# Performance work log

Hardware: AMD Instinct MI355X
Metric: run time of the kernel (lower is better)

## Reference

```python
import jax, jax.numpy as jnp
import numpy as np

N_PAPER = 50000
N_AUTHOR = 50000
E = 400000
N_FEAT = 256
N_HID = 256
N_CLASS = 128
TEMP = 1.0  # cfg.temparature


def setup_inputs() -> dict:
    key = jax.random.key(0)
    ks = jax.random.split(key, 40)
    def lin_init(k, shape, fan_in):
        s = 1.0 / np.sqrt(fan_in)
        return jax.random.uniform(k, shape, jnp.float32, -s, s)
    inp = {}
    inp['x_paper'] = jax.random.normal(ks[0], (N_PAPER, N_FEAT), jnp.float32)
    # xavier-uniform embedding for featureless node type 'author'
    xs = np.sqrt(6.0 / (N_AUTHOR + N_FEAT))
    inp['emb_author'] = jax.random.uniform(ks[1], (N_AUTHOR, N_FEAT), jnp.float32, -xs, xs)
    i = 2
    for l, fin in [(0, N_FEAT), (1, N_HID)]:
        for nt in ['paper', 'author']:
            inp[f'l{l}_root_{nt}_W'] = lin_init(ks[i], (fin, N_HID), fin); i += 1
            inp[f'l{l}_root_{nt}_b'] = lin_init(ks[i], (N_HID,), fin); i += 1
        for et in ['writes', 'rev', 'cites']:
            inp[f'l{l}_rel_{et}_W'] = lin_init(ks[i], (fin, N_HID), fin); i += 1
    inp['out_W'] = lin_init(ks[i], (N_HID, N_CLASS), N_HID); i += 1
    inp['out_b'] = lin_init(ks[i], (N_CLASS,), N_HID); i += 1
    inp['writes_src'] = jax.random.randint(ks[i], (E,), 0, N_AUTHOR); i += 1
    inp['writes_dst'] = jax.random.randint(ks[i], (E,), 0, N_PAPER); i += 1
    inp['rev_src'] = jax.random.randint(ks[i], (E,), 0, N_PAPER); i += 1
    inp['rev_dst'] = jax.random.randint(ks[i], (E,), 0, N_AUTHOR); i += 1
    inp['cites_src'] = jax.random.randint(ks[i], (E,), 0, N_PAPER); i += 1
    inp['cites_dst'] = jax.random.randint(ks[i], (E,), 0, N_PAPER); i += 1
    return inp


def _mean_agg(x_src, src, dst, n_dst):
    # sparse adj_t.matmul(x, reduce='mean'): segment-sum of gathered rows / in-degree (0 for isolated)
    msg = jax.ops.segment_sum(x_src[src], dst, num_segments=n_dst)  # [n_dst, d]
    deg = jax.ops.segment_sum(jnp.ones(src.shape[0], x_src.dtype), dst, num_segments=n_dst)
    return jnp.where(deg[:, None] > 0, msg / jnp.maximum(deg, 1.0)[:, None], 0.0)


def reference(x_paper, emb_author,
              l0_root_paper_W, l0_root_paper_b, l0_root_author_W, l0_root_author_b,
              l0_rel_writes_W, l0_rel_rev_W, l0_rel_cites_W,
              l1_root_paper_W, l1_root_paper_b, l1_root_author_W, l1_root_author_b,
              l1_rel_writes_W, l1_rel_rev_W, l1_rel_cites_W,
              out_W, out_b,
              writes_src, writes_dst, rev_src, rev_dst, cites_src, cites_dst):
    nnodes = {'paper': x_paper.shape[0], 'author': emb_author.shape[0]}
    # (src_type, dst_type, src_idx, dst_idx, rel_slot)
    edges = [('author', 'paper', writes_src, writes_dst, 0),
             ('paper', 'author', rev_src, rev_dst, 1),
             ('paper', 'paper', cites_src, cites_dst, 2)]
    layers = [
        {'root': {'paper': (l0_root_paper_W, l0_root_paper_b), 'author': (l0_root_author_W, l0_root_author_b)},
         'rel': [l0_rel_writes_W, l0_rel_rev_W, l0_rel_cites_W]},
        {'root': {'paper': (l1_root_paper_W, l1_root_paper_b), 'author': (l1_root_author_W, l1_root_author_b)},
         'rel': [l1_rel_writes_W, l1_rel_rev_W, l1_rel_cites_W]},
    ]
    xd = {'paper': x_paper, 'author': emb_author}
    xd_ = dict(xd)  # twin path starts from same features
    hs, hs_ = [], []
    for p in layers:
        out = {k: xd[k] @ p['root'][k][0] + p['root'][k][1] for k in xd}
        out_ = {k: xd_[k] @ p['root'][k][0] + p['root'][k][1] for k in xd_}
        for s, d, src, dst, slot in edges:
            W = p['rel'][slot]
            out[d] = out[d] + _mean_agg(xd[s], src, dst, nnodes[d]) @ W
            out_[d] = out_[d] + xd_[d] @ W  # twin path: no propagation, same rel transform
        xd = {k: jax.nn.relu(v) for k, v in out.items()}   # dropout is identity (eval)
        xd_ = {k: jax.nn.relu(v) for k, v in out_.items()}
        hs.append(xd['paper'])
        hs_.append(xd_['paper'])
    # Summarize: per-node dot-product attention over layer representations
    H = jnp.stack(hs)    # [L, N, d]
    H_ = jnp.stack(hs_)  # [L, N, d]
    alpha = jax.nn.softmax(jnp.sum(H * H_, axis=-1) / TEMP, axis=0)  # [L, N]
    h = jnp.sum(alpha[..., None] * H, axis=0)  # [N, d]
    logits = h @ out_W + out_b
    return (logits, alpha)
```

## Files before the change

### kernel.cpp

```cpp
#include <hip/hip_runtime.h>
#include <hip/hip_bf16.h>

#define NFEAT 256

typedef __attribute__((ext_vector_type(8))) short bf16x8;
typedef __attribute__((ext_vector_type(4))) float f32x4;
typedef __attribute__((ext_vector_type(8))) unsigned short us8;

__device__ __forceinline__ float bf2f(unsigned short u) {
    union { unsigned int i; float f; } v; v.i = ((unsigned int)u) << 16; return v.f;
}

__device__ __forceinline__ void f2hilo(float x, unsigned short& h, unsigned short& l) {
    __hip_bfloat16 hb = __float2bfloat16(x);
    float hf = __bfloat162float(hb);
    __hip_bfloat16 lb = __float2bfloat16(x - hf);
    h = *reinterpret_cast<unsigned short*>(&hb);
    l = *reinterpret_cast<unsigned short*>(&lb);
}

__global__ __launch_bounds__(256) void cvt8_kernel(
    const float* w0, const float* w1, const float* w2, const float* w3,
    const float* w4, const float* w5, const float* w6, const float* w7,
    unsigned short* base)
{
    int wi = blockIdx.y;
    const float* W = (wi==0)?w0:(wi==1)?w1:(wi==2)?w2:(wi==3)?w3:
                     (wi==4)?w4:(wi==5)?w5:(wi==6)?w6:w7;
    int idx = blockIdx.x * 256 + threadIdx.x;
    int k = idx >> 8, c = idx & 255;
    unsigned short h, l;
    f2hilo(W[idx], h, l);
    unsigned short* Th = base + (size_t)wi * 131072;
    Th[c * 256 + k] = h;
    Th[65536 + c * 256 + k] = l;
}

__global__ __launch_bounds__(256) void cvtfold_kernel(
    const float* a0, const float* a1, const float* a2,
    const float* b0, const float* b1, const float* b2,
    unsigned short* base)
{
    int wi = blockIdx.y;
    int idx = blockIdx.x * 256 + threadIdx.x;
    float v = wi ? (b0[idx] + b1[idx] + b2[idx]) : (a0[idx] + a1[idx] + a2[idx]);
    int k = idx >> 8, c = idx & 255;
    unsigned short h, l;
    f2hilo(v, h, l);
    unsigned short* Th = base + (size_t)(8 + wi) * 131072;
    Th[c * 256 + k] = h;
    Th[65536 + c * 256 + k] = l;
}

__global__ __launch_bounds__(256) void cvtrect_kernel(const float* W, unsigned short* base) {
    int idx = blockIdx.x * 256 + threadIdx.x;
    if (idx >= 256 * 128) return;
    int k = idx >> 7, c = idx & 127;
    unsigned short h, l;
    f2hilo(W[idx], h, l);
    unsigned short* Th = base + (size_t)10 * 131072;
    Th[c * 256 + k] = h;
    Th[65536 + c * 256 + k] = l;
}

__global__ __launch_bounds__(256) void deg_int_kernel(const int* __restrict__ dst,
                                                      int* __restrict__ deg, int nE) {
    int e = blockIdx.x * 256 + threadIdx.x;
    if (e < nE) atomicAdd(&deg[dst[e]], 1);
}

__global__ __launch_bounds__(256) void scan_p1(const int* __restrict__ deg, int n,
                                               int* __restrict__ off, int* __restrict__ bsum) {
    __shared__ int tmp[256];
    int tid = threadIdx.x;
    int i = blockIdx.x * 256 + tid;
    tmp[tid] = (i < n) ? deg[i] : 0;
    __syncthreads();
    #pragma unroll
    for (int ofs = 1; ofs < 256; ofs <<= 1) {
        int t = (tid >= ofs) ? tmp[tid - ofs] : 0;
        __syncthreads();
        tmp[tid] += t;
        __syncthreads();
    }
    if (i < n) off[i + 1] = tmp[tid];
    if (tid == 255) bsum[blockIdx.x] = tmp[255];
}

__global__ __launch_bounds__(256) void scan_p2(int* __restrict__ bA, int nA,
                                               int* __restrict__ bB, int nB,
                                               int* __restrict__ bC, int nC) {
    int* bs; int nb;
    if (blockIdx.x == 0) { bs = bA; nb = nA; }
    else if (blockIdx.x == 1) { bs = bB; nb = nB; }
    else { bs = bC; nb = nC; }
    __shared__ int tmp[256];
    int tid = threadIdx.x;
    tmp[tid] = (tid < nb) ? bs[tid] : 0;
    __syncthreads();
    #pragma unroll
    for (int ofs = 1; ofs < 256; ofs <<= 1) {
        int t = (tid >= ofs) ? tmp[tid - ofs] : 0;
        __syncthreads();
        tmp[tid] += t;
        __syncthreads();
    }
    if (tid < nb) bs[tid] = tmp[tid];
}

__global__ __launch_bounds__(256) void scan_p3(int n, int* __restrict__ off,
                                               const int* __restrict__ bsum) {
    int i = blockIdx.x * 256 + threadIdx.x;
    if (i == 0) off[0] = 0;
    if (i >= n) return;
    int b = blockIdx.x;
    if (b > 0) off[i + 1] += bsum[b - 1];
}

__global__ __launch_bounds__(256) void fill_csr_kernel(const int* __restrict__ src,
                                                       const int* __restrict__ dst, int nE,
                                                       const int* __restrict__ off,
                                                       int* __restrict__ cursor,
                                                       int* __restrict__ list) {
    int e = blockIdx.x * 256 + threadIdx.x;
    if (e >= nE) return;
    int d = dst[e];
    int pos = atomicAdd(&cursor[d], 1);
    list[off[d] + pos] = src[e];
}

__global__ __launch_bounds__(256) void agg_csr_kernel(const float* __restrict__ T,
                                                      const int* __restrict__ off,
                                                      const int* __restrict__ list,
                                                      float* __restrict__ D,
                                                      int mode_add, int do_relu, int M) {
    int r = blockIdx.x * 4 + (threadIdx.x >> 6);
    if (r >= M) return;
    int lane = threadIdx.x & 63;
    int start = off[r], end = off[r + 1];
    float4 acc = make_float4(0.f, 0.f, 0.f, 0.f);
    for (int e = start; e < end; ++e) {
        int s = list[e];
        float4 v = ((const float4*)(T + (size_t)s * NFEAT))[lane];
        acc.x += v.x; acc.y += v.y; acc.z += v.z; acc.w += v.w;
    }
    int cnt = end - start;
    float inv = (cnt > 0) ? 1.0f / (float)cnt : 0.0f;
    float4 d;
    if (mode_add) {
        d = ((float4*)(D + (size_t)r * NFEAT))[lane];
        d.x += acc.x * inv; d.y += acc.y * inv;
        d.z += acc.z * inv; d.w += acc.w * inv;
    } else {
        d.x = acc.x * inv; d.y = acc.y * inv;
        d.z = acc.z * inv; d.w = acc.w * inv;
    }
    if (do_relu) {
        d.x = fmaxf(d.x, 0.f); d.y = fmaxf(d.y, 0.f);
        d.z = fmaxf(d.z, 0.f); d.w = fmaxf(d.w, 0.f);
    }
    ((float4*)(D + (size_t)r * NFEAT))[lane] = d;
}

__global__ __launch_bounds__(256) void alpha_kernel(const float* __restrict__ s0,
                                                    const float* __restrict__ s1,
                                                    float* __restrict__ alpha, int M) {
    int n = blockIdx.x * 256 + threadIdx.x;
    if (n >= M) return;
    float v0 = s0[n], v1 = s1[n];
    float m = fmaxf(v0, v1);
    float e0 = expf(v0 - m), e1 = expf(v1 - m);
    float inv = 1.0f / (e0 + e1);
    alpha[n]     = e0 * inv;
    alpha[M + n] = e1 * inv;
}

struct Seg3 {
    const float *A0, *A1, *A2;
    const unsigned short *Wh0, *Wl0, *Wh1, *Wl1, *Wh2, *Wl2;
};

__global__ __launch_bounds__(256, 2) void gemm_ms(
    Seg3 sp, int nseg, const float* __restrict__ bias, int do_relu,
    float* __restrict__ C, int M, int N)
{
    __shared__ unsigned short Ah[128][40];
    __shared__ unsigned short Al[128][40];
    __shared__ unsigned short Bh[128][40];
    __shared__ unsigned short Bl[128][40];

    int tid = threadIdx.x;
    int lane = tid & 63;
    int w = tid >> 6;
    int wr = w >> 1, wc = w & 1;
    int row0 = blockIdx.x * 128, col0 = blockIdx.y * 128;
    int sr = tid >> 1;
    int sk = (tid & 1) * 16;
    int grow = row0 + sr; if (grow >= M) grow = M - 1;
    int fr = lane & 15;
    int fg = lane >> 4;

    f32x4 acc[4][4];
    #pragma unroll
    for (int m = 0; m < 4; ++m)
        #pragma unroll
        for (int n = 0; n < 4; ++n)
            acc[m][n] = (f32x4)(0.f);

    for (int s = 0; s < 3; ++s) {
        if (s >= nseg) break;
        const float* Xrow = ((s == 0) ? sp.A0 : (s == 1) ? sp.A1 : sp.A2) + (size_t)grow * NFEAT;
        const unsigned short* Whrow = ((s == 0) ? sp.Wh0 : (s == 1) ? sp.Wh1 : sp.Wh2) + (size_t)(col0 + sr) * NFEAT;
        const unsigned short* Wlrow = ((s == 0) ? sp.Wl0 : (s == 1) ? sp.Wl1 : sp.Wl2) + (size_t)(col0 + sr) * NFEAT;

        for (int k0 = 0; k0 < NFEAT; k0 += 32) {
            unsigned short hh[16], ll[16];
            #pragma unroll
            for (int q = 0; q < 4; ++q) {
                float4 v = *(const float4*)(Xrow + k0 + sk + q * 4);
                f2hilo(v.x, hh[q*4+0], ll[q*4+0]);
                f2hilo(v.y, hh[q*4+1], ll[q*4+1]);
                f2hilo(v.z, hh[q*4+2], ll[q*4+2]);
                f2hilo(v.w, hh[q*4+3], ll[q*4+3]);
            }
            us8 bh0 = *(const us8*)(Whrow + k0 + sk);
            us8 bh1 = *(const us8*)(Whrow + k0 + sk + 8);
            us8 bl0 = *(const us8*)(Wlrow + k0 + sk);
            us8 bl1 = *(const us8*)(Wlrow + k0 + sk + 8);
            __syncthreads();
            *(us8*)&Ah[sr][sk]     = *(us8*)&hh[0];
            *(us8*)&Ah[sr][sk + 8] = *(us8*)&hh[8];
            *(us8*)&Al[sr][sk]     = *(us8*)&ll[0];
            *(us8*)&Al[sr][sk + 8] = *(us8*)&ll[8];
            *(us8*)&Bh[sr][sk]     = bh0;
            *(us8*)&Bh[sr][sk + 8] = bh1;
            *(us8*)&Bl[sr][sk]     = bl0;
            *(us8*)&Bl[sr][sk + 8] = bl1;
            __syncthreads();

            bf16x8 ah[4], al[4], bhf[4], blf[4];
            #pragma unroll
            for (int m = 0; m < 4; ++m) {
                int r = wr * 64 + m * 16 + fr;
                ah[m] = *(const bf16x8*)&Ah[r][fg * 8];
                al[m] = *(const bf16x8*)&Al[r][fg * 8];
            }
            #pragma unroll
            for (int n = 0; n < 4; ++n) {
                int c = wc * 64 + n * 16 + fr;
                bhf[n] = *(const bf16x8*)&Bh[c][fg * 8];
                blf[n] = *(const bf16x8*)&Bl[c][fg * 8];
            }
            #pragma unroll
            for (int m = 0; m < 4; ++m)
                #pragma unroll
                for (int n = 0; n < 4; ++n) {
                    acc[m][n] = __builtin_amdgcn_mfma_f32_16x16x32_bf16(ah[m], bhf[n], acc[m][n], 0, 0, 0);
                    acc[m][n] = __builtin_amdgcn_mfma_f32_16x16x32_bf16(al[m], bhf[n], acc[m][n], 0, 0, 0);
                    acc[m][n] = __builtin_amdgcn_mfma_f32_16x16x32_bf16(ah[m], blf[n], acc[m][n], 0, 0, 0);
                }
        }
    }

    #pragma unroll
    for (int n = 0; n < 4; ++n) {
        int c = col0 + wc * 64 + n * 16 + fr;
        float bv = bias ? bias[c] : 0.f;
        #pragma unroll
        for (int m = 0; m < 4; ++m) {
            int rbase = row0 + wr * 64 + m * 16 + fg * 4;
            #pragma unroll
            for (int i = 0; i < 4; ++i) {
                int r = rbase + i;
                if (r < M) {
                    float v = acc[m][n][i] + bv;
                    if (do_relu) v = fmaxf(v, 0.f);
                    C[(size_t)r * N + c] = v;
                }
            }
        }
    }
}

__global__ __launch_bounds__(256, 2) void gemm_rowdot_mfma(
    const float* __restrict__ X,
    const unsigned short* __restrict__ Wh, const unsigned short* __restrict__ Wl,
    const float* __restrict__ bias,
    const float* __restrict__ P, const float* __restrict__ Q,
    float* __restrict__ s0g, float* __restrict__ s1g, int M)
{
    __shared__ unsigned short Ah[128][40];
    __shared__ unsigned short Al[128][40];
    __shared__ unsigned short Bh[128][40];
    __shared__ unsigned short Bl[128][40];
    __shared__ float srow[128];

    int tid = threadIdx.x;
    int lane = tid & 63;
    int w = tid >> 6;
    int wr = w >> 1, wc = w & 1;
    int row0 = blockIdx.x * 128;
    int sr = tid >> 1;
    int sk = (tid & 1) * 16;
    int grow = row0 + sr; if (grow >= M) grow = M - 1;
    int fr = lane & 15;
    int fg = lane >> 4;

    const float* Xrow = X + (size_t)grow * NFEAT;
    const float* Qrow = Q + (size_t)grow * NFEAT;

    if (tid < 128) srow[tid] = 0.f;
    float s0part = 0.f;
    float rp[4][4];
    #pragma unroll
    for (int m = 0; m < 4; ++m)
        #pragma unroll
        for (int i = 0; i < 4; ++i) rp[m][i] = 0.f;

    for (int ct = 0; ct < 2; ++ct) {
        int col0 = ct * 128;
        const unsigned short* Whrow = Wh + (size_t)(col0 + sr) * NFEAT;
        const unsigned short* Wlrow = Wl + (size_t)(col0 + sr) * NFEAT;

        f32x4 acc[4][4];
        #pragma unroll
        for (int m = 0; m < 4; ++m)
            #pragma unroll
            for (int n = 0; n < 4; ++n)
                acc[m][n] = (f32x4)(0.f);

        for (int k0 = 0; k0 < NFEAT; k0 += 32) {
            unsigned short hh[16], ll[16];
            #pragma unroll
            for (int q = 0; q < 4; ++q) {
                float4 v = *(const float4*)(Xrow + k0 + sk + q * 4);
                if (ct == 0) {
                    float4 qv = *(const float4*)(Qrow + k0 + sk + q * 4);
                    s0part += v.x * qv.x + v.y * qv.y + v.z * qv.z + v.w * qv.w;
                }
                f2hilo(v.x, hh[q*4+0], ll[q*4+0]);
                f2hilo(v.y, hh[q*4+1], ll[q*4+1]);
                f2hilo(v.z, hh[q*4+2], ll[q*4+2]);
                f2hilo(v.w, hh[q*4+3], ll[q*4+3]);
            }
            us8 bh0 = *(const us8*)(Whrow + k0 + sk);
            us8 bh1 = *(const us8*)(Whrow + k0 + sk + 8);
            us8 bl0 = *(const us8*)(Wlrow + k0 + sk);
            us8 bl1 = *(const us8*)(Wlrow + k0 + sk + 8);
            __syncthreads();
            *(us8*)&Ah[sr][sk]     = *(us8*)&hh[0];
            *(us8*)&Ah[sr][sk + 8] = *(us8*)&hh[8];
            *(us8*)&Al[sr][sk]     = *(us8*)&ll[0];
            *(us8*)&Al[sr][sk + 8] = *(us8*)&ll[8];
            *(us8*)&Bh[sr][sk]     = bh0;
            *(us8*)&Bh[sr][sk + 8] = bh1;
            *(us8*)&Bl[sr][sk]     = bl0;
            *(us8*)&Bl[sr][sk + 8] = bl1;
            __syncthreads();

            bf16x8 ah[4], al[4], bhf[4], blf[4];
            #pragma unroll
            for (int m = 0; m < 4; ++m) {
                int r = wr * 64 + m * 16 + fr;
                ah[m] = *(const bf16x8*)&Ah[r][fg * 8];
                al[m] = *(const bf16x8*)&Al[r][fg * 8];
            }
            #pragma unroll
            for (int n = 0; n < 4; ++n) {
                int c = wc * 64 + n * 16 + fr;
                bhf[n] = *(const bf16x8*)&Bh[c][fg * 8];
                blf[n] = *(const bf16x8*)&Bl[c][fg * 8];
            }
            #pragma unroll
            for (int m = 0; m < 4; ++m)
                #pragma unroll
                for (int n = 0; n < 4; ++n) {
                    acc[m][n] = __builtin_amdgcn_mfma_f32_16x16x32_bf16(ah[m], bhf[n], acc[m][n], 0, 0, 0);
                    acc[m][n] = __builtin_amdgcn_mfma_f32_16x16x32_bf16(al[m], bhf[n], acc[m][n], 0, 0, 0);
                    acc[m][n] = __builtin_amdgcn_mfma_f32_16x16x32_bf16(ah[m], blf[n], acc[m][n], 0, 0, 0);
                }
        }

        #pragma unroll
        for (int n = 0; n < 4; ++n) {
            int c = col0 + wc * 64 + n * 16 + fr;
            float bv = bias[c];
            #pragma unroll
            for (int m = 0; m < 4; ++m) {
                #pragma unroll
                for (int i = 0; i < 4; ++i) {
                    int r = row0 + wr * 64 + m * 16 + fg * 4 + i;
                    if (r < M) {
                        float v = fmaxf(acc[m][n][i] + bv, 0.f);
                        rp[m][i] += v * P[(size_t)r * NFEAT + c];
                    }
                }
            }
        }
    }

    #pragma unroll
    for (int o = 1; o < 16; o <<= 1) {
        #pragma unroll
        for (int m = 0; m < 4; ++m)
            #pragma unroll
            for (int i = 0; i < 4; ++i)
                rp[m][i] += __shfl_xor(rp[m][i], o);
    }
    if ((lane & 15) == 0) {
        #pragma unroll
        for (int m = 0; m < 4; ++m)
            #pragma unroll
            for (int i = 0; i < 4; ++i)
                atomicAdd(&srow[wr * 64 + m * 16 + fg * 4 + i], rp[m][i]);
    }
    s0part += __shfl_xor(s0part, 1);
    if ((tid & 1) == 0 && row0 + sr < M) s0g[row0 + sr] = s0part;
    __syncthreads();
    if (tid < 128 && row0 + tid < M) s1g[row0 + tid] = srow[tid];
}

__global__ __launch_bounds__(256, 2) void gemm_head(
    const float* __restrict__ P1, const float* __restrict__ P2,
    const float* __restrict__ alpha,
    const unsigned short* __restrict__ Wh, const unsigned short* __restrict__ Wl,
    const float* __restrict__ bias,
    float* __restrict__ C, int M, int N)
{
    __shared__ unsigned short Ah[128][40];
    __shared__ unsigned short Al[128][40];
    __shared__ unsigned short Bh[128][40];
    __shared__ unsigned short Bl[128][40];

    int tid = threadIdx.x;
    int lane = tid & 63;
    int w = tid >> 6;
    int wr = w >> 1, wc = w & 1;
    int row0 = blockIdx.x * 128;
    int sr = tid >> 1;
    int sk = (tid & 1) * 16;
    int grow = row0 + sr; if (grow >= M) grow = M - 1;
    int fr = lane & 15;
    int fg = lane >> 4;

    const float* P1row = P1 + (size_t)grow * NFEAT;
    const float* P2row = P2 + (size_t)grow * NFEAT;
    float a0 = alpha[grow], a1 = alpha[M + grow];

    f32x4 acc[4][4];
    #pragma unroll
    for (int m = 0; m < 4; ++m)
        #pragma unroll
        for (int n = 0; n < 4; ++n)
            acc[m][n] = (f32x4)(0.f);

    const unsigned short* Whrow = Wh + (size_t)sr * NFEAT;
    const unsigned short* Wlrow = Wl + (size_t)sr * NFEAT;

    for (int k0 = 0; k0 < NFEAT; k0 += 32) {
        unsigned short hh[16], ll[16];
        #pragma unroll
        for (int q = 0; q < 4; ++q) {
            float4 v1 = *(const float4*)(P1row + k0 + sk + q * 4);
            float4 v2 = *(const float4*)(P2row + k0 + sk + q * 4);
            float4 v = make_float4(a0 * v1.x + a1 * v2.x, a0 * v1.y + a1 * v2.y,
                                   a0 * v1.z + a1 * v2.z, a0 * v1.w + a1 * v2.w);
            f2hilo(v.x, hh[q*4+0], ll[q*4+0]);
            f2hilo(v.y, hh[q*4+1], ll[q*4+1]);
            f2hilo(v.z, hh[q*4+2], ll[q*4+2]);
            f2hilo(v.w, hh[q*4+3], ll[q*4+3]);
        }
        us8 bh0 = *(const us8*)(Whrow + k0 + sk);
        us8 bh1 = *(const us8*)(Whrow + k0 + sk + 8);
        us8 bl0 = *(const us8*)(Wlrow + k0 + sk);
        us8 bl1 = *(const us8*)(Wlrow + k0 + sk + 8);
        __syncthreads();
        *(us8*)&Ah[sr][sk]     = *(us8*)&hh[0];
        *(us8*)&Ah[sr][sk + 8] = *(us8*)&hh[8];
        *(us8*)&Al[sr][sk]     = *(us8*)&ll[0];
        *(us8*)&Al[sr][sk + 8] = *(us8*)&ll[8];
        *(us8*)&Bh[sr][sk]     = bh0;
        *(us8*)&Bh[sr][sk + 8] = bh1;
        *(us8*)&Bl[sr][sk]     = bl0;
        *(us8*)&Bl[sr][sk + 8] = bl1;
        __syncthreads();

        bf16x8 ah[4], al[4], bhf[4], blf[4];
        #pragma unroll
        for (int m = 0; m < 4; ++m) {
            int r = wr * 64 + m * 16 + fr;
            ah[m] = *(const bf16x8*)&Ah[r][fg * 8];
            al[m] = *(const bf16x8*)&Al[r][fg * 8];
        }
        #pragma unroll
        for (int n = 0; n < 4; ++n) {
            int c = wc * 64 + n * 16 + fr;
            bhf[n] = *(const bf16x8*)&Bh[c][fg * 8];
            blf[n] = *(const bf16x8*)&Bl[c][fg * 8];
        }
        #pragma unroll
        for (int m = 0; m < 4; ++m)
            #pragma unroll
            for (int n = 0; n < 4; ++n) {
                acc[m][n] = __builtin_amdgcn_mfma_f32_16x16x32_bf16(ah[m], bhf[n], acc[m][n], 0, 0, 0);
                acc[m][n] = __builtin_amdgcn_mfma_f32_16x16x32_bf16(al[m], bhf[n], acc[m][n], 0, 0, 0);
                acc[m][n] = __builtin_amdgcn_mfma_f32_16x16x32_bf16(ah[m], blf[n], acc[m][n], 0, 0, 0);
            }
    }

    #pragma unroll
    for (int n = 0; n < 4; ++n) {
        int c = wc * 64 + n * 16 + fr;
        if (c >= N) continue;
        float bv = bias[c];
        #pragma unroll
        for (int m = 0; m < 4; ++m) {
            int rbase = row0 + wr * 64 + m * 16 + fg * 4;
            #pragma unroll
            for (int i = 0; i < 4; ++i) {
                int r = rbase + i;
                if (r < M) C[(size_t)r * N + c] = acc[m][n][i] + bv;
            }
        }
    }
}

extern "C" void kernel_launch(void* const* d_in, const int* in_sizes, int n_in,
                              void* d_out, int out_size, void* d_ws, size_t ws_size,
                              hipStream_t stream)
{
    const float* x_paper    = (const float*)d_in[0];
    const float* emb_author = (const float*)d_in[1];
    const float* W0rp = (const float*)d_in[2];
    const float* b0rp = (const float*)d_in[3];
    const float* W0ra = (const float*)d_in[4];
    const float* b0ra = (const float*)d_in[5];
    const float* W0w  = (const float*)d_in[6];
    const float* W0rev= (const float*)d_in[7];
    const float* W0c  = (const float*)d_in[8];
    const float* W1rp = (const float*)d_in[9];
    const float* b1rp = (const float*)d_in[10];
    const float* W1w  = (const float*)d_in[13];
    const float* W1c  = (const float*)d_in[15];
    const float* outW = (const float*)d_in[16];
    const float* outb = (const float*)d_in[17];
    const int* w_src = (const int*)d_in[18];
    const int* w_dst = (const int*)d_in[19];
    const int* r_src = (const int*)d_in[20];
    const int* r_dst = (const int*)d_in[21];
    const int* c_src = (const int*)d_in[22];
    const int* c_dst = (const int*)d_in[23];

    const int NP = in_sizes[0] / NFEAT;
    const int NA = in_sizes[1] / NFEAT;
    const int NC = in_sizes[17];
    const int nEw = in_sizes[18], nEr = in_sizes[20], nEc = in_sizes[22];

    size_t NB = (size_t)(NP > NA ? NP : NA) * NFEAT;
    float* Z0 = (float*)d_ws;
    float* Z1 = Z0 + NB;
    float* Z2 = Z1 + NB;
    float* s0 = Z2 + NB;
    float* s1 = s0 + NP;
    unsigned short* Wt = (unsigned short*)(s1 + NP);
    #define WT_HI(i) (Wt + (size_t)(i) * 131072)
    #define WT_LO(i) (Wt + (size_t)(i) * 131072 + 65536)
    int* degW = (int*)(Wt + 11 * 131072);
    int* degR = degW + NP;
    int* degC = degR + NA;
    int* curW = degC + NP;
    int* curR = curW + NP;
    int* curC = curR + NA;
    int* offW = curC + NP;
    int* offR = offW + NP + 1;
    int* offC = offR + NA + 1;
    int* bsW  = offC + NP + 1;
    int* bsR  = bsW + 256;
    int* bsC  = bsR + 256;
    int* listW = bsC + 256;
    int* listR = listW + nEw;
    int* listC = listR + nEr;

    float* out   = (float*)d_out;
    float* alpha = out + (size_t)NP * NC;

    hipMemsetAsync(degW, 0, (size_t)2 * (NP + NA + NP) * sizeof(int), stream);
    deg_int_kernel<<<(nEw + 255) / 256, 256, 0, stream>>>(w_dst, degW, nEw);
    deg_int_kernel<<<(nEr + 255) / 256, 256, 0, stream>>>(r_dst, degR, nEr);
    deg_int_kernel<<<(nEc + 255) / 256, 256, 0, stream>>>(c_dst, degC, nEc);

    int nbP = (NP + 255) / 256, nbA = (NA + 255) / 256;
    scan_p1<<<nbP, 256, 0, stream>>>(degW, NP, offW, bsW);
    scan_p1<<<nbA, 256, 0, stream>>>(degR, NA, offR, bsR);
    scan_p1<<<nbP, 256, 0, stream>>>(degC, NP, offC, bsC);
    scan_p2<<<3, 256, 0, stream>>>(bsW, nbP, bsR, nbA, bsC, nbP);
    scan_p3<<<nbP, 256, 0, stream>>>(NP, offW, bsW);
    scan_p3<<<nbA, 256, 0, stream>>>(NA, offR, bsR);
    scan_p3<<<nbP, 256, 0, stream>>>(NP, offC, bsC);

    fill_csr_kernel<<<(nEw + 255) / 256, 256, 0, stream>>>(w_src, w_dst, nEw, offW, curW, listW);
    fill_csr_kernel<<<(nEr + 255) / 256, 256, 0, stream>>>(r_src, r_dst, nEr, offR, curR, listR);
    fill_csr_kernel<<<(nEc + 255) / 256, 256, 0, stream>>>(c_src, c_dst, nEc, offC, curC, listC);

    cvt8_kernel<<<dim3(256, 8), 256, 0, stream>>>(W0rp, W0w, W0c, W0ra, W0rev, W1rp, W1w, W1c, Wt);
    cvtfold_kernel<<<dim3(256, 2), 256, 0, stream>>>(W0rp, W0w, W0c, W1rp, W1w, W1c, Wt);
    cvtrect_kernel<<<128, 256, 0, stream>>>(outW, Wt);

    dim3 blk(256);
    dim3 gP((NP + 127) / 128, 2);
    dim3 gA((NA + 127) / 128, 2);
    dim3 g1((NP + 127) / 128);
    int nodeP = (NP + 3) / 4, nodeA = (NA + 3) / 4;

    agg_csr_kernel<<<nodeP, blk, 0, stream>>>(emb_author, offW, listW, Z0, 0, 0, NP);
    agg_csr_kernel<<<nodeP, blk, 0, stream>>>(x_paper,    offC, listC, Z1, 0, 0, NP);
    {
        Seg3 sp = {x_paper, Z0, Z1, WT_HI(0), WT_LO(0), WT_HI(1), WT_LO(1), WT_HI(2), WT_LO(2)};
        gemm_ms<<<gP, blk, 0, stream>>>(sp, 3, b0rp, 1, Z2, NP, NFEAT);
    }
    agg_csr_kernel<<<nodeA, blk, 0, stream>>>(x_paper, offR, listR, Z0, 0, 0, NA);
    {
        Seg3 sp = {emb_author, Z0, nullptr, WT_HI(3), WT_LO(3), WT_HI(4), WT_LO(4), nullptr, nullptr};
        gemm_ms<<<gA, blk, 0, stream>>>(sp, 2, b0ra, 1, Z1, NA, NFEAT);
    }

    agg_csr_kernel<<<nodeP, blk, 0, stream>>>(Z1, offW, listW, Z0, 0, 0, NP);
    {
        Seg3 sp = {Z2, Z0, nullptr, WT_HI(5), WT_LO(5), WT_HI(6), WT_LO(6), nullptr, nullptr};
        gemm_ms<<<gP, blk, 0, stream>>>(sp, 2, b1rp, 0, Z1, NP, NFEAT);
    }
    {
        Seg3 sp = {Z2, nullptr, nullptr, WT_HI(7), WT_LO(7), nullptr, nullptr, nullptr, nullptr};
        gemm_ms<<<gP, blk, 0, stream>>>(sp, 1, nullptr, 0, Z0, NP, NFEAT);
    }
    agg_csr_kernel<<<nodeP, blk, 0, stream>>>(Z0, offC, listC, Z1, 1, 1, NP);

    {
        Seg3 sp = {x_paper, nullptr, nullptr, WT_HI(8), WT_LO(8), nullptr, nullptr, nullptr, nullptr};
        gemm_ms<<<gP, blk, 0, stream>>>(sp, 1, b0rp, 1, Z0, NP, NFEAT);
    }
    gemm_rowdot_mfma<<<g1, blk, 0, stream>>>(Z0, WT_HI(9), WT_LO(9), b1rp, Z1, Z2, s0, s1, NP);

    alpha_kernel<<<(NP + 255) / 256, blk, 0, stream>>>(s0, s1, alpha, NP);
    gemm_head<<<g1, blk, 0, stream>>>(Z2, Z1, alpha, WT_HI(10), WT_LO(10), outb, out, NP, NC);
}
```

Before: 879.3 us.

## Load MFMA fragments directly from global memory, dropping LDS staging

```diff
diff --git a/kernel.cpp b/kernel.cpp
--- a/kernel.cpp
+++ b/kernel.cpp
@@ -17,6 +17,19 @@
     __hip_bfloat16 lb = __float2bfloat16(x - hf);
     h = *reinterpret_cast<unsigned short*>(&hb);
     l = *reinterpret_cast<unsigned short*>(&lb);
+}
+
+__device__ __forceinline__ void load_frag_f32(const float* __restrict__ p,
+                                              bf16x8& h, bf16x8& l) {
+    float4 x0 = *(const float4*)p;
+    float4 x1 = *(const float4*)(p + 4);
+    float xs[8] = {x0.x, x0.y, x0.z, x0.w, x1.x, x1.y, x1.z, x1.w};
+    #pragma unroll
+    for (int j = 0; j < 8; ++j) {
+        unsigned short hh, ll;
+        f2hilo(xs[j], hh, ll);
+        h[j] = (short)hh; l[j] = (short)ll;
+    }
 }
 
 __global__ __launch_bounds__(256) void cvt8_kernel(
@@ -184,22 +197,23 @@
     Seg3 sp, int nseg, const float* __restrict__ bias, int do_relu,
     float* __restrict__ C, int M, int N)
 {
-    __shared__ unsigned short Ah[128][40];
-    __shared__ unsigned short Al[128][40];
-    __shared__ unsigned short Bh[128][40];
-    __shared__ unsigned short Bl[128][40];
-
     int tid = threadIdx.x;
     int lane = tid & 63;
     int w = tid >> 6;
     int wr = w >> 1, wc = w & 1;
     int row0 = blockIdx.x * 128, col0 = blockIdx.y * 128;
-    int sr = tid >> 1;
-    int sk = (tid & 1) * 16;
-    int grow = row0 + sr; if (grow >= M) grow = M - 1;
     int fr = lane & 15;
     int fg = lane >> 4;
 
+    int rowm[4], coln[4];
+    #pragma unroll
+    for (int m = 0; m < 4; ++m) {
+        int r = row0 + wr * 64 + m * 16 + fr;
+        rowm[m] = (r < M) ? r : (M - 1);
+    }
+    #pragma unroll
+    for (int n = 0; n < 4; ++n) coln[n] = col0 + wc * 64 + n * 16 + fr;
+
     f32x4 acc[4][4];
     #pragma unroll
     for (int m = 0; m < 4; ++m)
@@ -209,55 +223,28 @@
 
     for (int s = 0; s < 3; ++s) {
         if (s >= nseg) break;
-        const float* Xrow = ((s == 0) ? sp.A0 : (s == 1) ? sp.A1 : sp.A2) + (size_t)grow * NFEAT;
-        const unsigned short* Whrow = ((s == 0) ? sp.Wh0 : (s == 1) ? sp.Wh1 : sp.Wh2) + (size_t)(col0 + sr) * NFEAT;
-        const unsigned short* Wlrow = ((s == 0) ? sp.Wl0 : (s == 1) ? sp.Wl1 : sp.Wl2) + (size_t)(col0 + sr) * NFEAT;
+        const float* A = (s == 0) ? sp.A0 : (s == 1) ? sp.A1 : sp.A2;
+        const unsigned short* Wh = (s == 0) ? sp.Wh0 : (s == 1) ? sp.Wh1 : sp.Wh2;
+        const unsigned short* Wl = (s == 0) ? sp.Wl0 : (s == 1) ? sp.Wl1 : sp.Wl2;
 
         for (int k0 = 0; k0 < NFEAT; k0 += 32) {
-            unsigned short hh[16], ll[16];
-            #pragma unroll
-            for (int q = 0; q < 4; ++q) {
-                float4 v = *(const float4*)(Xrow + k0 + sk + q * 4);
-                f2hilo(v.x, hh[q*4+0], ll[q*4+0]);
-                f2hilo(v.y, hh[q*4+1], ll[q*4+1]);
-                f2hilo(v.z, hh[q*4+2], ll[q*4+2]);
-                f2hilo(v.w, hh[q*4+3], ll[q*4+3]);
-            }
-            us8 bh0 = *(const us8*)(Whrow + k0 + sk);
-            us8 bh1 = *(const us8*)(Whrow + k0 + sk + 8);
-            us8 bl0 = *(const us8*)(Wlrow + k0 + sk);
-            us8 bl1 = *(const us8*)(Wlrow + k0 + sk + 8);
-            __syncthreads();
-            *(us8*)&Ah[sr][sk]     = *(us8*)&hh[0];
-            *(us8*)&Ah[sr][sk + 8] = *(us8*)&hh[8];
-            *(us8*)&Al[sr][sk]     = *(us8*)&ll[0];
-            *(us8*)&Al[sr][sk + 8] = *(us8*)&ll[8];
-            *(us8*)&Bh[sr][sk]     = bh0;
-            *(us8*)&Bh[sr][sk + 8] = bh1;
-            *(us8*)&Bl[sr][sk]     = bl0;
-            *(us8*)&Bl[sr][sk + 8] = bl1;
-            __syncthreads();
-
-            bf16x8 ah[4], al[4], bhf[4], blf[4];
-            #pragma unroll
-            for (int m = 0; m < 4; ++m) {
-                int r = wr * 64 + m * 16 + fr;
-                ah[m] = *(const bf16x8*)&Ah[r][fg * 8];
-                al[m] = *(const bf16x8*)&Al[r][fg * 8];
-            }
+            bf16x8 ah[4], al[4], bh[4], bl[4];
+            #pragma unroll
+            for (int m = 0; m < 4; ++m)
+                load_frag_f32(A + (size_t)rowm[m] * NFEAT + k0 + fg * 8, ah[m], al[m]);
             #pragma unroll
             for (int n = 0; n < 4; ++n) {
-                int c = wc * 64 + n * 16 + fr;
-                bhf[n] = *(const bf16x8*)&Bh[c][fg * 8];
-                blf[n] = *(const bf16x8*)&Bl[c][fg * 8];
+                size_t wo = (size_t)coln[n] * NFEAT + k0 + fg * 8;
+                bh[n] = *reinterpret_cast<const bf16x8*>(Wh + wo);
+                bl[n] = *reinterpret_cast<const bf16x8*>(Wl + wo);
             }
             #pragma unroll
             for (int m = 0; m < 4; ++m)
                 #pragma unroll
                 for (int n = 0; n < 4; ++n) {
-                    acc[m][n] = __builtin_amdgcn_mfma_f32_16x16x32_bf16(ah[m], bhf[n], acc[m][n], 0, 0, 0);
-                    acc[m][n] = __builtin_amdgcn_mfma_f32_16x16x32_bf16(al[m], bhf[n], acc[m][n], 0, 0, 0);
-                    acc[m][n] = __builtin_amdgcn_mfma_f32_16x16x32_bf16(ah[m], blf[n], acc[m][n], 0, 0, 0);
+                    acc[m][n] = __builtin_amdgcn_mfma_f32_16x16x32_bf16(ah[m], bh[n], acc[m][n], 0, 0, 0);
+                    acc[m][n] = __builtin_amdgcn_mfma_f32_16x16x32_bf16(al[m], bh[n], acc[m][n], 0, 0, 0);
+                    acc[m][n] = __builtin_amdgcn_mfma_f32_16x16x32_bf16(ah[m], bl[n], acc[m][n], 0, 0, 0);
                 }
         }
     }
@@ -289,10 +276,6 @@
     const float* __restrict__ P, const float* __restrict__ Q,
     float* __restrict__ s0g, float* __restrict__ s1g, int M)
 {
-    __shared__ unsigned short Ah[128][40];
-    __shared__ unsigned short Al[128][40];
-    __shared__ unsigned short Bh[128][40];
-    __shared__ unsigned short Bl[128][40];
     __shared__ float srow[128];
 
     int tid = threadIdx.x;
@@ -300,17 +283,20 @@
     int w = tid >> 6;
     int wr = w >> 1, wc = w & 1;
     int row0 = blockIdx.x * 128;
-    int sr = tid >> 1;
-    int sk = (tid & 1) * 16;
-    int grow = row0 + sr; if (grow >= M) grow = M - 1;
     int fr = lane & 15;
     int fg = lane >> 4;
 
-    const float* Xrow = X + (size_t)grow * NFEAT;
-    const float* Qrow = Q + (size_t)grow * NFEAT;
-
     if (tid < 128) srow[tid] = 0.f;
-    float s0part = 0.f;
+    __syncthreads();
+
+    int rowm[4];
+    #pragma unroll
+    for (int m = 0; m < 4; ++m) {
+        int r = row0 + wr * 64 + m * 16 + fr;
+        rowm[m] = (r < M) ? r : (M - 1);
+    }
+
+    float s0p[4] = {0.f, 0.f, 0.f, 0.f};
     float rp[4][4];
     #pragma unroll
     for (int m = 0; m < 4; ++m)
@@ -319,8 +305,9 @@
 
     for (int ct = 0; ct < 2; ++ct) {
         int col0 = ct * 128;
-        const unsigned short* Whrow = Wh + (size_t)(col0 + sr) * NFEAT;
-        const unsigned short* Wlrow = Wl + (size_t)(col0 + sr) * NFEAT;
+        int coln[4];
+        #pragma unroll
+        for (int n = 0; n < 4; ++n) coln[n] = col0 + wc * 64 + n * 16 + fr;
 
         f32x4 acc[4][4];
         #pragma unroll
@@ -330,60 +317,46 @@
                 acc[m][n] = (f32x4)(0.f);
 
         for (int k0 = 0; k0 < NFEAT; k0 += 32) {
-            unsigned short hh[16], ll[16];
-            #pragma unroll
-            for (int q = 0; q < 4; ++q) {
-                float4 v = *(const float4*)(Xrow + k0 + sk + q * 4);
+            bf16x8 ah[4], al[4], bh[4], bl[4];
+            #pragma unroll
+            for (int m = 0; m < 4; ++m) {
+                const float* pa = X + (size_t)rowm[m] * NFEAT + k0 + fg * 8;
+                float4 x0 = *(const float4*)pa;
+                float4 x1 = *(const float4*)(pa + 4);
                 if (ct == 0) {
-                    float4 qv = *(const float4*)(Qrow + k0 + sk + q * 4);
-                    s0part += v.x * qv.x + v.y * qv.y + v.z * qv.z + v.w * qv.w;
+                    const float* pq = Q + (size_t)rowm[m] * NFEAT + k0 + fg * 8;
+                    float4 q0 = *(const float4*)pq;
+                    float4 q1 = *(const float4*)(pq + 4);
+                    s0p[m] += x0.x*q0.x + x0.y*q0.y + x0.z*q0.z + x0.w*q0.w
+                            + x1.x*q1.x + x1.y*q1.y + x1.z*q1.z + x1.w*q1.w;
                 }
-                f2hilo(v.x, hh[q*4+0], ll[q*4+0]);
-                f2hilo(v.y, hh[q*4+1], ll[q*4+1]);
-                f2hilo(v.z, hh[q*4+2], ll[q*4+2]);
-                f2hilo(v.w, hh[q*4+3], ll[q*4+3]);
-            }
-            us8 bh0 = *(const us8*)(Whrow + k0 + sk);
-            us8 bh1 = *(const us8*)(Whrow + k0 + sk + 8);
-            us8 bl0 = *(const us8*)(Wlrow + k0 + sk);
-            us8 bl1 = *(const us8*)(Wlrow + k0 + sk + 8);
-            __syncthreads();
-            *(us8*)&Ah[sr][sk]     = *(us8*)&hh[0];
-            *(us8*)&Ah[sr][sk + 8] = *(us8*)&hh[8];
-            *(us8*)&Al[sr][sk]     = *(us8*)&ll[0];
-            *(us8*)&Al[sr][sk + 8] = *(us8*)&ll[8];
-            *(us8*)&Bh[sr][sk]     = bh0;
-            *(us8*)&Bh[sr][sk + 8] = bh1;
-            *(us8*)&Bl[sr][sk]     = bl0;
-            *(us8*)&Bl[sr][sk + 8] = bl1;
-            __syncthreads();
-
-            bf16x8 ah[4], al[4], bhf[4], blf[4];
-            #pragma unroll
-            for (int m = 0; m < 4; ++m) {
-                int r = wr * 64 + m * 16 + fr;
-                ah[m] = *(const bf16x8*)&Ah[r][fg * 8];
-                al[m] = *(const bf16x8*)&Al[r][fg * 8];
+                float xs[8] = {x0.x, x0.y, x0.z, x0.w, x1.x, x1.y, x1.z, x1.w};
+                #pragma unroll
+                for (int j = 0; j < 8; ++j) {
+                    unsigned short hh, ll;
+                    f2hilo(xs[j], hh, ll);
+                    ah[m][j] = (short)hh; al[m][j] = (short)ll;
+                }
             }
             #pragma unroll
             for (int n = 0; n < 4; ++n) {
-                int c = wc * 64 + n * 16 + fr;
-                bhf[n] = *(const bf16x8*)&Bh[c][fg * 8];
-                blf[n] = *(const bf16x8*)&Bl[c][fg * 8];
+                size_t wo = (size_t)coln[n] * NFEAT + k0 + fg * 8;
+                bh[n] = *reinterpret_cast<const bf16x8*>(Wh + wo);
+                bl[n] = *reinterpret_cast<const bf16x8*>(Wl + wo);
             }
             #pragma unroll
             for (int m = 0; m < 4; ++m)
                 #pragma unroll
                 for (int n = 0; n < 4; ++n) {
-                    acc[m][n] = __builtin_amdgcn_mfma_f32_16x16x32_bf16(ah[m], bhf[n], acc[m][n], 0, 0, 0);
-                    acc[m][n] = __builtin_amdgcn_mfma_f32_16x16x32_bf16(al[m], bhf[n], acc[m][n], 0, 0, 0);
-                    acc[m][n] = __builtin_amdgcn_mfma_f32_16x16x32_bf16(ah[m], blf[n], acc[m][n], 0, 0, 0);
+                    acc[m][n] = __builtin_amdgcn_mfma_f32_16x16x32_bf16(ah[m], bh[n], acc[m][n], 0, 0, 0);
+                    acc[m][n] = __builtin_amdgcn_mfma_f32_16x16x32_bf16(al[m], bh[n], acc[m][n], 0, 0, 0);
+                    acc[m][n] = __builtin_amdgcn_mfma_f32_16x16x32_bf16(ah[m], bl[n], acc[m][n], 0, 0, 0);
                 }
         }
 
         #pragma unroll
         for (int n = 0; n < 4; ++n) {
-            int c = col0 + wc * 64 + n * 16 + fr;
+            int c = coln[n];
             float bv = bias[c];
             #pragma unroll
             for (int m = 0; m < 4; ++m) {
@@ -400,6 +373,19 @@
     }
 
     #pragma unroll
+    for (int m = 0; m < 4; ++m) {
+        s0p[m] += __shfl_xor(s0p[m], 16);
+        s0p[m] += __shfl_xor(s0p[m], 32);
+    }
+    if (wc == 0 && lane < 16) {
+        #pragma unroll
+        for (int m = 0; m < 4; ++m) {
+            int r = row0 + wr * 64 + m * 16 + lane;
+            if (r < M) s0g[r] = s0p[m];
+        }
+    }
+
+    #pragma unroll
     for (int o = 1; o < 16; o <<= 1) {
         #pragma unroll
         for (int m = 0; m < 4; ++m)
@@ -414,8 +400,6 @@
             for (int i = 0; i < 4; ++i)
                 atomicAdd(&srow[wr * 64 + m * 16 + fg * 4 + i], rp[m][i]);
     }
-    s0part += __shfl_xor(s0part, 1);
-    if ((tid & 1) == 0 && row0 + sr < M) s0g[row0 + sr] = s0part;
     __syncthreads();
     if (tid < 128 && row0 + tid < M) s1g[row0 + tid] = srow[tid];
 }
@@ -427,25 +411,25 @@
     const float* __restrict__ bias,
     float* __restrict__ C, int M, int N)
 {
-    __shared__ unsigned short Ah[128][40];
-    __shared__ unsigned short Al[128][40];
-    __shared__ unsigned short Bh[128][40];
-    __shared__ unsigned short Bl[128][40];
-
     int tid = threadIdx.x;
     int lane = tid & 63;
     int w = tid >> 6;
     int wr = w >> 1, wc = w & 1;
     int row0 = blockIdx.x * 128;
-    int sr = tid >> 1;
-    int sk = (tid & 1) * 16;
-    int grow = row0 + sr; if (grow >= M) grow = M - 1;
     int fr = lane & 15;
     int fg = lane >> 4;
 
-    const float* P1row = P1 + (size_t)grow * NFEAT;
-    const float* P2row = P2 + (size_t)grow * NFEAT;
-    float a0 = alpha[grow], a1 = alpha[M + grow];
+    int rowm[4], coln[4];
+    float a0m[4], a1m[4];
+    #pragma unroll
+    for (int m = 0; m < 4; ++m) {
+        int r = row0 + wr * 64 + m * 16 + fr;
+        rowm[m] = (r < M) ? r : (M - 1);
+        a0m[m] = alpha[rowm[m]];
+        a1m[m] = alpha[M + rowm[m]];
+    }
+    #pragma unroll
+    for (int n = 0; n < 4; ++n) coln[n] = wc * 64 + n * 16 + fr;
 
     f32x4 acc[4][4];
     #pragma unroll
@@ -454,63 +438,46 @@
         for (int n = 0; n < 4; ++n)
             acc[m][n] = (f32x4)(0.f);
 
-    const unsigned short* Whrow = Wh + (size_t)sr * NFEAT;
-    const unsigned short* Wlrow = Wl + (size_t)sr * NFEAT;
-
     for (int k0 = 0; k0 < NFEAT; k0 += 32) {
-        unsigned short hh[16], ll[16];
-        #pragma unroll
-        for (int q = 0; q < 4; ++q) {
-            float4 v1 = *(const float4*)(P1row + k0 + sk + q * 4);
-            float4 v2 = *(const float4*)(P2row + k0 + sk + q * 4);
-            float4 v = make_float4(a0 * v1.x + a1 * v2.x, a0 * v1.y + a1 * v2.y,
-                                   a0 * v1.z + a1 * v2.z, a0 * v1.w + a1 * v2.w);
-            f2hilo(v.x, hh[q*4+0], ll[q*4+0]);
-            f2hilo(v.y, hh[q*4+1], ll[q*4+1]);
-            f2hilo(v.z, hh[q*4+2], ll[q*4+2]);
-            f2hilo(v.w, hh[q*4+3], ll[q*4+3]);
-        }
-        us8 bh0 = *(const us8*)(Whrow + k0 + sk);
-        us8 bh1 = *(const us8*)(Whrow + k0 + sk + 8);
-        us8 bl0 = *(const us8*)(Wlrow + k0 + sk);
-        us8 bl1 = *(const us8*)(Wlrow + k0 + sk + 8);
-        __syncthreads();
-        *(us8*)&Ah[sr][sk]     = *(us8*)&hh[0];
-        *(us8*)&Ah[sr][sk + 8] = *(us8*)&hh[8];
-        *(us8*)&Al[sr][sk]     = *(us8*)&ll[0];
-        *(us8*)&Al[sr][sk + 8] = *(us8*)&ll[8];
-        *(us8*)&Bh[sr][sk]     = bh0;
-        *(us8*)&Bh[sr][sk + 8] = bh1;
-        *(us8*)&Bl[sr][sk]     = bl0;
-        *(us8*)&Bl[sr][sk + 8] = bl1;
-        __syncthreads();
-
-        bf16x8 ah[4], al[4], bhf[4], blf[4];
+        bf16x8 ah[4], al[4], bh[4], bl[4];
         #pragma unroll
         for (int m = 0; m < 4; ++m) {
-            int r = wr * 64 + m * 16 + fr;
-            ah[m] = *(const bf16x8*)&Ah[r][fg * 8];
-            al[m] = *(const bf16x8*)&Al[r][fg * 8];
+            const float* p1 = P1 + (size_t)rowm[m] * NFEAT + k0 + fg * 8;
+            const float* p2 = P2 + (size_t)rowm[m] * NFEAT + k0 + fg * 8;
+            float4 u0 = *(const float4*)p1;
+            float4 u1 = *(const float4*)(p1 + 4);
+            float4 v0 = *(const float4*)p2;
+            float4 v1 = *(const float4*)(p2 + 4);
+            float xs[8] = {a0m[m]*u0.x + a1m[m]*v0.x, a0m[m]*u0.y + a1m[m]*v0.y,
+                           a0m[m]*u0.z + a1m[m]*v0.z, a0m[m]*u0.w + a1m[m]*v0.w,
+                           a0m[m]*u1.x + a1m[m]*v1.x, a0m[m]*u1.y + a1m[m]*v1.y,
+                           a0m[m]*u1.z + a1m[m]*v1.z, a0m[m]*u1.w + a1m[m]*v1.w};
+            #pragma unroll
+            for (int j = 0; j < 8; ++j) {
+                unsigned short hh, ll;
+                f2hilo(xs[j], hh, ll);
+                ah[m][j] = (short)hh; al[m][j] = (short)ll;
+            }
         }
         #pragma unroll
         for (int n = 0; n < 4; ++n) {
-            int c = wc * 64 + n * 16 + fr;
-            bhf[n] = *(const bf16x8*)&Bh[c][fg * 8];
-            blf[n] = *(const bf16x8*)&Bl[c][fg * 8];
+            size_t wo = (size_t)coln[n] * NFEAT + k0 + fg * 8;
+            bh[n] = *reinterpret_cast<const bf16x8*>(Wh + wo);
+            bl[n] = *reinterpret_cast<const bf16x8*>(Wl + wo);
         }
         #pragma unroll
         for (int m = 0; m < 4; ++m)
             #pragma unroll
             for (int n = 0; n < 4; ++n) {
-                acc[m][n] = __builtin_amdgcn_mfma_f32_16x16x32_bf16(ah[m], bhf[n], acc[m][n], 0, 0, 0);
-                acc[m][n] = __builtin_amdgcn_mfma_f32_16x16x32_bf16(al[m], bhf[n], acc[m][n], 0, 0, 0);
-                acc[m][n] = __builtin_amdgcn_mfma_f32_16x16x32_bf16(ah[m], blf[n], acc[m][n], 0, 0, 0);
+                acc[m][n] = __builtin_amdgcn_mfma_f32_16x16x32_bf16(ah[m], bh[n], acc[m][n], 0, 0, 0);
+                acc[m][n] = __builtin_amdgcn_mfma_f32_16x16x32_bf16(al[m], bh[n], acc[m][n], 0, 0, 0);
+                acc[m][n] = __builtin_amdgcn_mfma_f32_16x16x32_bf16(ah[m], bl[n], acc[m][n], 0, 0, 0);
             }
     }
 
     #pragma unroll
     for (int n = 0; n < 4; ++n) {
-        int c = wc * 64 + n * 16 + fr;
+        int c = coln[n];
         if (c >= N) continue;
         float bv = bias[c];
         #pragma unroll
```

After: 1.338 ms. 52.1% more time.
